# Kernel tuning notes

Hardware: AMD Instinct MI355X
Metric: run time of the kernel (lower is better)

Reference implementation:

```python
import jax, jax.numpy as jnp
import numpy as np

NUM_LAYER = 5
EMB = 64
ATOM_F = 32
BOND_F = 16
N_NODES = 50000
N_EDGES = 800000


def mish(x):
    return x * jnp.tanh(jax.nn.softplus(x))


def setup_inputs() -> dict:
    key = jax.random.key(0)
    ks = jax.random.split(key, 12)
    x = jax.random.normal(ks[0], (N_NODES, ATOM_F), dtype=jnp.float32)
    edge_index = jax.random.randint(ks[1], (2, N_EDGES), 0, N_NODES, dtype=jnp.int32)
    edge_attr = jax.random.normal(ks[2], (N_EDGES, BOND_F), dtype=jnp.float32)
    s = 0.05
    Wemb = jax.random.normal(ks[3], (EMB, ATOM_F), dtype=jnp.float32) * s
    W1 = jax.random.normal(ks[4], (NUM_LAYER, 2 * EMB, EMB), dtype=jnp.float32) * s
    b1 = jnp.zeros((NUM_LAYER, 2 * EMB), dtype=jnp.float32)
    W2 = jax.random.normal(ks[5], (NUM_LAYER, EMB, 2 * EMB), dtype=jnp.float32) * s
    b2 = jnp.zeros((NUM_LAYER, EMB), dtype=jnp.float32)
    We = jax.random.normal(ks[6], (NUM_LAYER, EMB, BOND_F), dtype=jnp.float32) * s
    be = jnp.zeros((NUM_LAYER, EMB), dtype=jnp.float32)
    gamma = jnp.ones((NUM_LAYER, EMB), dtype=jnp.float32)
    beta = jnp.zeros((NUM_LAYER, EMB), dtype=jnp.float32)
    return {"x": x, "edge_attr": edge_attr, "Wemb": Wemb, "W1": W1, "b1": b1,
            "W2": W2, "b2": b2, "We": We, "be": be, "gamma": gamma,
            "beta": beta, "edge_index": edge_index}


def reference(x, edge_attr, Wemb, W1, b1, W2, b2, We, be, gamma, beta, edge_index):
    N = x.shape[0]
    num_layer = W1.shape[0]
    # x_embedding: Linear(atom_feat, emb, bias=False)
    h = x @ Wemb.T  # [N, EMB]
    # add self loops once (edge_index is identical per layer in the module)
    loop = jnp.arange(N, dtype=edge_index.dtype)
    src = jnp.concatenate([edge_index[0], loop])  # message source (x_j)
    dst = jnp.concatenate([edge_index[1], loop])  # aggregation target
    # self-loop edge_attr is zeros
    ea_full = jnp.concatenate(
        [edge_attr, jnp.zeros((N, edge_attr.shape[1]), edge_attr.dtype)], axis=0)
    for l in range(num_layer):
        # GINConv: edge embedding + gather + scatter-add + MLP
        ee = ea_full @ We[l].T + be[l]          # [E+N, EMB]
        msg = h[src] + ee                        # x_j + edge_attr
        aggr = jax.ops.segment_sum(msg, dst, num_segments=N)  # aggr='add'
        hid = jax.nn.relu(aggr @ W1[l].T + b1[l])
        hn = hid @ W2[l].T + b2[l]
        # BatchNorm1d (training mode: batch statistics, biased variance)
        mu = hn.mean(axis=0)
        var = hn.var(axis=0)
        hn = (hn - mu) * jax.lax.rsqrt(var + 1e-5) * gamma[l] + beta[l]
        # mish on all but last layer; drop_ratio=0 so dropout is identity
        if l < num_layer - 1:
            hn = mish(hn)
        h = hn
    # JK='last'
    return h
```

## Files before the change

kernel.cpp:

```cpp
#include <hip/hip_runtime.h>

#define EMB 64
#define HID 128
#define BONDF 16
#define ATOMF 32

typedef __attribute__((ext_vector_type(8))) short short8v;
typedef __attribute__((ext_vector_type(16))) float f32x16;

__device__ __forceinline__ unsigned short f32_to_bf16_rne(float f) {
  unsigned u = __float_as_uint(f);
  u = (u + 0x7FFFu + ((u >> 16) & 1u)) >> 16;
  return (unsigned short)u;
}

__global__ __launch_bounds__(256) void embed_kernel(
    const float* __restrict__ x, const float* __restrict__ Wemb,
    float* __restrict__ h, int N)
{
  __shared__ float sW[EMB * ATOMF];
  int tid = threadIdx.x;
  for (int i = tid; i < EMB * ATOMF; i += 256) sW[i] = Wemb[i];
  __syncthreads();
  int row = blockIdx.x * 256 + tid;
  if (row >= N) return;
  float xin[ATOMF];
  const float4* xr = reinterpret_cast<const float4*>(x + (size_t)row * ATOMF);
#pragma unroll
  for (int k4 = 0; k4 < ATOMF / 4; ++k4) {
    float4 v = xr[k4];
    xin[4 * k4 + 0] = v.x; xin[4 * k4 + 1] = v.y;
    xin[4 * k4 + 2] = v.z; xin[4 * k4 + 3] = v.w;
  }
  float4* hr = reinterpret_cast<float4*>(h + (size_t)row * EMB);
  for (int o4 = 0; o4 < EMB / 4; ++o4) {
    float acc[4];
#pragma unroll
    for (int c = 0; c < 4; ++c) {
      const float* wrow = sW + (o4 * 4 + c) * ATOMF;
      float a = 0.f;
#pragma unroll
      for (int kk = 0; kk < ATOMF / 4; ++kk) {
        float4 w = reinterpret_cast<const float4*>(wrow)[kk];
        a = fmaf(w.x, xin[4 * kk + 0], a);
        a = fmaf(w.y, xin[4 * kk + 1], a);
        a = fmaf(w.z, xin[4 * kk + 2], a);
        a = fmaf(w.w, xin[4 * kk + 3], a);
      }
      acc[c] = a;
    }
    hr[o4] = make_float4(acc[0], acc[1], acc[2], acc[3]);
  }
}

__global__ __launch_bounds__(256) void cvt_bf16_kernel(
    const float* __restrict__ s, unsigned short* __restrict__ d, int n)
{
  int i = blockIdx.x * 256 + threadIdx.x;
  if (i < n) d[i] = f32_to_bf16_rne(s[i]);
}

__global__ __launch_bounds__(256) void deg_kernel(
    const int* __restrict__ ei, int* __restrict__ deg, int E)
{
  int e = blockIdx.x * 256 + threadIdx.x;
  if (e < E) atomicAdd(&deg[ei[E + e]], 1);
}

__global__ __launch_bounds__(256) void scan1_kernel(
    const int* __restrict__ deg, int* __restrict__ off,
    int* __restrict__ bsum, int n)
{
  __shared__ int ws[4];
  int tid = threadIdx.x, lane = tid & 63, wid = tid >> 6;
  int i = blockIdx.x * 256 + tid;
  int v = (i < n) ? deg[i] : 0;
  int x = v;
#pragma unroll
  for (int d = 1; d < 64; d <<= 1) {
    int t = __shfl_up(x, d, 64);
    if (lane >= d) x += t;
  }
  if (lane == 63) ws[wid] = x;
  __syncthreads();
  int add = 0;
  for (int w = 0; w < wid; ++w) add += ws[w];
  if (i < n) off[i] = x + add - v;
  if (tid == 255) bsum[blockIdx.x] = x + add;
}

__global__ __launch_bounds__(256) void scan_small_kernel(
    const int* __restrict__ deg, int* __restrict__ off, int n)
{
  __shared__ int warpsums[4];
  __shared__ int s_carry;
  int tid = threadIdx.x, lane = tid & 63, wid = tid >> 6;
  if (tid == 0) s_carry = 0;
  __syncthreads();
  for (int base = 0; base < n; base += 256) {
    int i = base + tid;
    int v = (i < n) ? deg[i] : 0;
    int x = v;
#pragma unroll
    for (int d = 1; d < 64; d <<= 1) {
      int t = __shfl_up(x, d, 64);
      if (lane >= d) x += t;
    }
    if (lane == 63) warpsums[wid] = x;
    __syncthreads();
    int wsum = 0;
    for (int w = 0; w < wid; ++w) wsum += warpsums[w];
    int incl = x + wsum + s_carry;
    if (i < n) off[i] = incl - v;
    __syncthreads();
    if (tid == 255) s_carry = incl;
    __syncthreads();
  }
  if (tid == 0) off[n] = s_carry;
}

__global__ __launch_bounds__(256) void scan3_kernel(
    int* __restrict__ off, const int* __restrict__ boff, int n)
{
  int i = blockIdx.x * 256 + threadIdx.x;
  if (i < n) off[i] += boff[blockIdx.x];
  if (i == 0) off[n] = boff[gridDim.x];
}

__global__ __launch_bounds__(256) void place_kernel(
    const int* __restrict__ ei, const int* __restrict__ off,
    int* __restrict__ cursor, int2* __restrict__ csr_packed, int E)
{
  int e = blockIdx.x * 256 + threadIdx.x;
  if (e >= E) return;
  int d = ei[E + e];
  int pos = atomicAdd(&cursor[d], 1);
  csr_packed[off[d] + pos] = make_int2(ei[e], e);
}

__global__ __launch_bounds__(256) void gather_ea_kernel(
    const float* __restrict__ ea, const int* __restrict__ off,
    const int2* __restrict__ csr_packed, float* __restrict__ S_ea, int N)
{
  int f = threadIdx.x & 15;
  int node = blockIdx.x * 16 + (threadIdx.x >> 4);
  if (node >= N) return;
  float acc = 0.f;
  int s0 = off[node], s1 = off[node + 1];
  int e = s0;
  if (e < s1 && (e & 1)) {
    acc += ea[(size_t)csr_packed[e].y * BONDF + f];
    ++e;
  }
  for (; e + 3 < s1; e += 4) {
    int4 p0 = *reinterpret_cast<const int4*>(csr_packed + e);
    int4 p1 = *reinterpret_cast<const int4*>(csr_packed + e + 2);
    float v0 = ea[(size_t)p0.y * BONDF + f];
    float v1 = ea[(size_t)p0.w * BONDF + f];
    float v2 = ea[(size_t)p1.y * BONDF + f];
    float v3 = ea[(size_t)p1.w * BONDF + f];
    acc += v0; acc += v1; acc += v2; acc += v3;
  }
  for (; e < s1; ++e)
    acc += ea[(size_t)csr_packed[e].y * BONDF + f];
  S_ea[(size_t)node * BONDF + f] = acc;
}

#define WEP (EMB + 1)
__global__ __launch_bounds__(256) void aggregate_ea_kernel(
    const float* __restrict__ h, const int* __restrict__ off,
    const int2* __restrict__ csr_packed, const float* __restrict__ S_ea,
    const float* __restrict__ We_l, const float* __restrict__ be_l,
    unsigned short* __restrict__ aggr16, int N)
{
  __shared__ float sWet[BONDF * WEP];
  __shared__ float sbe[EMB];
  int tid = threadIdx.x;
  for (int i = tid; i < EMB * BONDF; i += 256) {
    int k = i >> 4, f = i & 15;
    sWet[f * WEP + k] = We_l[i];
  }
  if (tid < EMB) sbe[tid] = be_l[tid];
  __syncthreads();
  int lane = tid & 63;
  int node = blockIdx.x * 4 + (tid >> 6);
  if (node >= N) return;
  float acc = h[(size_t)node * EMB + lane];
  int s0 = off[node], s1 = off[node + 1];
  int e = s0;
  if (e < s1 && (e & 1)) {
    acc += h[(size_t)csr_packed[e].x * EMB + lane];
    ++e;
  }
  for (; e + 15 < s1; e += 16) {
    int4 p0 = *reinterpret_cast<const int4*>(csr_packed + e);
    int4 p1 = *reinterpret_cast<const int4*>(csr_packed + e + 2);
    int4 p2 = *reinterpret_cast<const int4*>(csr_packed + e + 4);
    int4 p3 = *reinterpret_cast<const int4*>(csr_packed + e + 6);
    int4 p4 = *reinterpret_cast<const int4*>(csr_packed + e + 8);
    int4 p5 = *reinterpret_cast<const int4*>(csr_packed + e + 10);
    int4 p6 = *reinterpret_cast<const int4*>(csr_packed + e + 12);
    int4 p7 = *reinterpret_cast<const int4*>(csr_packed + e + 14);
    float v0  = h[(size_t)p0.x * EMB + lane];
    float v1  = h[(size_t)p0.z * EMB + lane];
    float v2  = h[(size_t)p1.x * EMB + lane];
    float v3  = h[(size_t)p1.z * EMB + lane];
    float v4  = h[(size_t)p2.x * EMB + lane];
    float v5  = h[(size_t)p2.z * EMB + lane];
    float v6  = h[(size_t)p3.x * EMB + lane];
    float v7  = h[(size_t)p3.z * EMB + lane];
    float v8  = h[(size_t)p4.x * EMB + lane];
    float v9  = h[(size_t)p4.z * EMB + lane];
    float v10 = h[(size_t)p5.x * EMB + lane];
    float v11 = h[(size_t)p5.z * EMB + lane];
    float v12 = h[(size_t)p6.x * EMB + lane];
    float v13 = h[(size_t)p6.z * EMB + lane];
    float v14 = h[(size_t)p7.x * EMB + lane];
    float v15 = h[(size_t)p7.z * EMB + lane];
    acc += v0;  acc += v1;  acc += v2;  acc += v3;
    acc += v4;  acc += v5;  acc += v6;  acc += v7;
    acc += v8;  acc += v9;  acc += v10; acc += v11;
    acc += v12; acc += v13; acc += v14; acc += v15;
  }
  for (; e + 1 < s1; e += 2) {
    int4 p = *reinterpret_cast<const int4*>(csr_packed + e);
    float v0 = h[(size_t)p.x * EMB + lane];
    float v1 = h[(size_t)p.z * EMB + lane];
    acc += v0; acc += v1;
  }
  if (e < s1) acc += h[(size_t)csr_packed[e].x * EMB + lane];
  float dp1 = (float)(s1 - s0) + 1.0f;
  acc = fmaf(sbe[lane], dp1, acc);
  const float* sea = S_ea + (size_t)node * BONDF;
#pragma unroll
  for (int f = 0; f < BONDF; ++f)
    acc = fmaf(sWet[f * WEP + lane], sea[f], acc);
  aggr16[(size_t)node * EMB + lane] = f32_to_bf16_rne(acc);
}

__global__ __launch_bounds__(256) void mlp_mfma_kernel(
    const unsigned short* __restrict__ aggr16,
    const unsigned short* __restrict__ W1b,
    const unsigned short* __restrict__ W2b,
    const float* __restrict__ b1,
    float* __restrict__ tmp, int N)
{
  int wid = threadIdx.x >> 6;
  int lane = threadIdx.x & 63;
  int chunk = blockIdx.x * 4 + wid;
  int row0 = chunk * 32;
  if (row0 >= N) return;
  int col = lane & 31;
  int g = lane >> 5;
  int row = row0 + col;
  int rowc = min(row, N - 1);

  f32x16 acc1[4] = {};
#pragma unroll
  for (int kt = 0; kt < 4; ++kt) {
    short8v bfrag = *reinterpret_cast<const short8v*>(
        aggr16 + (size_t)rowc * EMB + kt * 16 + g * 8);
#pragma unroll
    for (int mt = 0; mt < 4; ++mt) {
      short8v afrag = *reinterpret_cast<const short8v*>(
          W1b + (size_t)(mt * 32 + col) * EMB + kt * 16 + g * 8);
      acc1[mt] = __builtin_amdgcn_mfma_f32_32x32x16_bf16(afrag, bfrag, acc1[mt], 0, 0, 0);
    }
  }

  unsigned u[32];
#pragma unroll
  for (int t = 0; t < 16; ++t) {
    const int mt = t >> 2, q = t & 3;
    float v0 = fmaxf(acc1[mt][4 * q + 0] + b1[mt * 32 + 8 * q + 4 * g + 0], 0.f);
    float v1 = fmaxf(acc1[mt][4 * q + 1] + b1[mt * 32 + 8 * q + 4 * g + 1], 0.f);
    float v2 = fmaxf(acc1[mt][4 * q + 2] + b1[mt * 32 + 8 * q + 4 * g + 2], 0.f);
    float v3 = fmaxf(acc1[mt][4 * q + 3] + b1[mt * 32 + 8 * q + 4 * g + 3], 0.f);
    asm("v_cvt_pk_bf16_f32 %0, %1, %2" : "=v"(u[2 * t + 0]) : "v"(v0), "v"(v1));
    asm("v_cvt_pk_bf16_f32 %0, %1, %2" : "=v"(u[2 * t + 1]) : "v"(v2), "v"(v3));
  }

  short8v b2f[8];
#pragma unroll
  for (int kt2 = 0; kt2 < 8; ++kt2) {
    unsigned e0 = u[4 * kt2 + 0], e1 = u[4 * kt2 + 1];
    unsigned o0 = u[4 * kt2 + 2], o1 = u[4 * kt2 + 3];
    unsigned pe0 = (unsigned)__shfl_xor((int)e0, 32, 64);
    unsigned pe1 = (unsigned)__shfl_xor((int)e1, 32, 64);
    unsigned po0 = (unsigned)__shfl_xor((int)o0, 32, 64);
    unsigned po1 = (unsigned)__shfl_xor((int)o1, 32, 64);
    union { unsigned w[4]; short8v v; } cvt;
    cvt.w[0] = (g == 0) ? e0 : po0;
    cvt.w[1] = (g == 0) ? e1 : po1;
    cvt.w[2] = (g == 0) ? pe0 : o0;
    cvt.w[3] = (g == 0) ? pe1 : o1;
    b2f[kt2] = cvt.v;
  }

  f32x16 acc2[2] = {};
#pragma unroll
  for (int kt2 = 0; kt2 < 8; ++kt2) {
#pragma unroll
    for (int mt2 = 0; mt2 < 2; ++mt2) {
      short8v a2 = *reinterpret_cast<const short8v*>(
          W2b + (size_t)(mt2 * 32 + col) * HID + kt2 * 16 + g * 8);
      acc2[mt2] = __builtin_amdgcn_mfma_f32_32x32x16_bf16(a2, b2f[kt2], acc2[mt2], 0, 0, 0);
    }
  }

  if (row < N) {
#pragma unroll
    for (int mt2 = 0; mt2 < 2; ++mt2)
#pragma unroll
      for (int r = 0; r < 16; ++r) {
        int o = mt2 * 32 + (r & 3) + 8 * (r >> 2) + 4 * g;
        tmp[(size_t)row * EMB + o] = acc2[mt2][r];
      }
  }
}

__global__ __launch_bounds__(256) void stats_kernel(
    const float* __restrict__ tmp, float* __restrict__ gsums, int N)
{
  __shared__ float sh[256], sh2[256];
  int tid = threadIdx.x;
  int c = tid & 63, rg = tid >> 6;
  float s = 0.f, s2 = 0.f;
  for (int r = blockIdx.x * 4 + rg; r < N; r += gridDim.x * 4) {
    float v = tmp[(size_t)r * EMB + c];
    s += v; s2 += v * v;
  }
  sh[tid] = s; sh2[tid] = s2;
  __syncthreads();
  if (tid < 64) {
    s = sh[tid] + sh[tid + 64] + sh[tid + 128] + sh[tid + 192];
    s2 = sh2[tid] + sh2[tid + 64] + sh2[tid + 128] + sh2[tid + 192];
    atomicAdd(&gsums[c], s);
    atomicAdd(&gsums[EMB + c], s2);
  }
}

__global__ __launch_bounds__(256) void bn_kernel(
    const float* __restrict__ tmp, const float* __restrict__ gsums,
    const float* __restrict__ gamma, const float* __restrict__ beta,
    float* __restrict__ out, int N, int apply_mish)
{
  int idx = blockIdx.x * 256 + threadIdx.x;
  int total = N * (EMB / 4);
  if (idx >= total) return;
  int c4 = idx & (EMB / 4 - 1);
  float invN = 1.0f / (float)N;
  float4 v = reinterpret_cast<const float4*>(tmp)[idx];
  float o[4] = {v.x, v.y, v.z, v.w};
#pragma unroll
  for (int c = 0; c < 4; ++c) {
    int col = c4 * 4 + c;
    float mu = gsums[col] * invN;
    float var = gsums[EMB + col] * invN - mu * mu;
    float sc = gamma[col] * rsqrtf(var + 1e-5f);
    float shf = beta[col] - mu * sc;
    float y = o[c] * sc + shf;
    if (apply_mish) {
      float sp = (y > 20.f) ? y : log1pf(expf(y));
      y = y * tanhf(sp);
    }
    o[c] = y;
  }
  reinterpret_cast<float4*>(out)[idx] = make_float4(o[0], o[1], o[2], o[3]);
}

extern "C" void kernel_launch(void* const* d_in, const int* in_sizes, int n_in,
                              void* d_out, int out_size, void* d_ws, size_t ws_size,
                              hipStream_t stream) {
  (void)n_in; (void)out_size; (void)ws_size;
  const float* x     = (const float*)d_in[0];
  const float* ea    = (const float*)d_in[1];
  const float* Wemb  = (const float*)d_in[2];
  const float* W1    = (const float*)d_in[3];
  const float* b1    = (const float*)d_in[4];
  const float* W2    = (const float*)d_in[5];
  const float* We    = (const float*)d_in[7];
  const float* be    = (const float*)d_in[8];
  const float* gamma = (const float*)d_in[9];
  const float* beta  = (const float*)d_in[10];
  const int*   ei    = (const int*)d_in[11];

  int N = in_sizes[0] / ATOMF;
  int E = in_sizes[11] / 2;
  int L = in_sizes[3] / (HID * EMB);

  char* w = (char*)d_ws;
  auto alloc = [&](size_t bytes) {
    void* p = (void*)w;
    w += (bytes + 255) & ~(size_t)255;
    return p;
  };
  float*          h      = (float*)alloc((size_t)N * EMB * 4);
  float*          tmp    = (float*)alloc((size_t)N * EMB * 4);
  unsigned short* aggr16 = (unsigned short*)alloc((size_t)N * EMB * 2);
  float*          S_ea   = (float*)alloc((size_t)N * BONDF * 4);
  int*            deg    = (int*)alloc((size_t)N * 4);
  int*            off    = (int*)alloc((size_t)(N + 1) * 4);
  int*            cursor = (int*)alloc((size_t)N * 4);
  int2*           csrp   = (int2*)alloc((size_t)E * 8);
  int*            bsum   = (int*)alloc(1024 * 4);
  int*            boff   = (int*)alloc(1025 * 4);
  float*          gsums  = (float*)alloc(2 * EMB * 4);
  unsigned short* W1b    = (unsigned short*)alloc((size_t)L * HID * EMB * 2);
  unsigned short* W2b    = (unsigned short*)alloc((size_t)L * HID * EMB * 2);

  hipMemsetAsync(deg, 0, (size_t)N * 4, stream);
  hipMemsetAsync(cursor, 0, (size_t)N * 4, stream);

  int nW = L * HID * EMB;
  cvt_bf16_kernel<<<(nW + 255) / 256, 256, 0, stream>>>(W1, W1b, nW);
  cvt_bf16_kernel<<<(nW + 255) / 256, 256, 0, stream>>>(W2, W2b, nW);

  int nb = (N + 255) / 256;
  deg_kernel<<<(E + 255) / 256, 256, 0, stream>>>(ei, deg, E);
  scan1_kernel<<<nb, 256, 0, stream>>>(deg, off, bsum, N);
  scan_small_kernel<<<1, 256, 0, stream>>>(bsum, boff, nb);
  scan3_kernel<<<nb, 256, 0, stream>>>(off, boff, N);
  place_kernel<<<(E + 255) / 256, 256, 0, stream>>>(ei, off, cursor, csrp, E);
  gather_ea_kernel<<<(N + 15) / 16, 256, 0, stream>>>(ea, off, csrp, S_ea, N);
  embed_kernel<<<(N + 255) / 256, 256, 0, stream>>>(x, Wemb, h, N);

  int nchunk = (N + 31) / 32;
  for (int l = 0; l < L; ++l) {
    aggregate_ea_kernel<<<(N + 3) / 4, 256, 0, stream>>>(
        h, off, csrp, S_ea, We + (size_t)l * EMB * BONDF, be + (size_t)l * EMB,
        aggr16, N);
    mlp_mfma_kernel<<<(nchunk + 3) / 4, 256, 0, stream>>>(
        aggr16, W1b + (size_t)l * HID * EMB, W2b + (size_t)l * HID * EMB,
        b1 + (size_t)l * HID, tmp, N);
    hipMemsetAsync(gsums, 0, 2 * EMB * 4, stream);
    stats_kernel<<<512, 256, 0, stream>>>(tmp, gsums, N);
    float* outp = (l == L - 1) ? (float*)d_out : h;
    bn_kernel<<<(N * (EMB / 4) + 255) / 256, 256, 0, stream>>>(
        tmp, gsums, gamma + (size_t)l * EMB, beta + (size_t)l * EMB,
        outp, N, (l < L - 1) ? 1 : 0);
  }
}
```

Baseline: 740.2 us.

## Fuse BatchNorm statistics into MLP kernel and vectorize edge placement

Computes the per-column sum and sum-of-squares for BatchNorm inside the MFMA MLP kernel, using shared-memory atomics and then one global atomic per column per block. This removes the separate stats kernel and its re-read of tmp. It also replaces the per-layer memset with a single up-front memset of per-layer stat buffers, and merges the deg/cursor memsets into one. The place kernel now handles four edges per thread using int4 loads. The cost is heavy LDS atomic contention (many lanes add into the same 64 columns) and more global atomics, since each of the roughly 390 blocks adds its partial sums.

```diff
diff --git a/kernel.cpp b/kernel.cpp
--- a/kernel.cpp
+++ b/kernel.cpp
@@ -131,11 +131,27 @@
     const int* __restrict__ ei, const int* __restrict__ off,
     int* __restrict__ cursor, int2* __restrict__ csr_packed, int E)
 {
-  int e = blockIdx.x * 256 + threadIdx.x;
-  if (e >= E) return;
-  int d = ei[E + e];
-  int pos = atomicAdd(&cursor[d], 1);
-  csr_packed[off[d] + pos] = make_int2(ei[e], e);
+  int t = blockIdx.x * 256 + threadIdx.x;
+  int e0 = t * 4;
+  if (e0 >= E) return;
+  if (e0 + 3 < E) {
+    int4 s = *reinterpret_cast<const int4*>(ei + e0);
+    int4 d = *reinterpret_cast<const int4*>(ei + E + e0);
+    int p0 = atomicAdd(&cursor[d.x], 1);
+    int p1 = atomicAdd(&cursor[d.y], 1);
+    int p2 = atomicAdd(&cursor[d.z], 1);
+    int p3 = atomicAdd(&cursor[d.w], 1);
+    csr_packed[off[d.x] + p0] = make_int2(s.x, e0 + 0);
+    csr_packed[off[d.y] + p1] = make_int2(s.y, e0 + 1);
+    csr_packed[off[d.z] + p2] = make_int2(s.z, e0 + 2);
+    csr_packed[off[d.w] + p3] = make_int2(s.w, e0 + 3);
+  } else {
+    for (int e = e0; e < E; ++e) {
+      int d = ei[E + e];
+      int pos = atomicAdd(&cursor[d], 1);
+      csr_packed[off[d] + pos] = make_int2(ei[e], e);
+    }
+  }
 }
 
 __global__ __launch_bounds__(256) void gather_ea_kernel(
@@ -243,101 +259,93 @@
     const unsigned short* __restrict__ W1b,
     const unsigned short* __restrict__ W2b,
     const float* __restrict__ b1,
-    float* __restrict__ tmp, int N)
-{
-  int wid = threadIdx.x >> 6;
-  int lane = threadIdx.x & 63;
+    float* __restrict__ tmp, float* __restrict__ gsums_l, int N)
+{
+  __shared__ float sstat[2 * EMB];
+  int tid = threadIdx.x;
+  for (int i = tid; i < 2 * EMB; i += 256) sstat[i] = 0.f;
+  __syncthreads();
+
+  int wid = tid >> 6;
+  int lane = tid & 63;
   int chunk = blockIdx.x * 4 + wid;
   int row0 = chunk * 32;
-  if (row0 >= N) return;
-  int col = lane & 31;
-  int g = lane >> 5;
-  int row = row0 + col;
-  int rowc = min(row, N - 1);
-
-  f32x16 acc1[4] = {};
-#pragma unroll
-  for (int kt = 0; kt < 4; ++kt) {
-    short8v bfrag = *reinterpret_cast<const short8v*>(
-        aggr16 + (size_t)rowc * EMB + kt * 16 + g * 8);
-#pragma unroll
-    for (int mt = 0; mt < 4; ++mt) {
-      short8v afrag = *reinterpret_cast<const short8v*>(
-          W1b + (size_t)(mt * 32 + col) * EMB + kt * 16 + g * 8);
-      acc1[mt] = __builtin_amdgcn_mfma_f32_32x32x16_bf16(afrag, bfrag, acc1[mt], 0, 0, 0);
-    }
-  }
-
-  unsigned u[32];
-#pragma unroll
-  for (int t = 0; t < 16; ++t) {
-    const int mt = t >> 2, q = t & 3;
-    float v0 = fmaxf(acc1[mt][4 * q + 0] + b1[mt * 32 + 8 * q + 4 * g + 0], 0.f);
-    float v1 = fmaxf(acc1[mt][4 * q + 1] + b1[mt * 32 + 8 * q + 4 * g + 1], 0.f);
-    float v2 = fmaxf(acc1[mt][4 * q + 2] + b1[mt * 32 + 8 * q + 4 * g + 2], 0.f);
-    float v3 = fmaxf(acc1[mt][4 * q + 3] + b1[mt * 32 + 8 * q + 4 * g + 3], 0.f);
-    asm("v_cvt_pk_bf16_f32 %0, %1, %2" : "=v"(u[2 * t + 0]) : "v"(v0), "v"(v1));
-    asm("v_cvt_pk_bf16_f32 %0, %1, %2" : "=v"(u[2 * t + 1]) : "v"(v2), "v"(v3));
-  }
-
-  short8v b2f[8];
-#pragma unroll
-  for (int kt2 = 0; kt2 < 8; ++kt2) {
-    unsigned e0 = u[4 * kt2 + 0], e1 = u[4 * kt2 + 1];
-    unsigned o0 = u[4 * kt2 + 2], o1 = u[4 * kt2 + 3];
-    unsigned pe0 = (unsigned)__shfl_xor((int)e0, 32, 64);
-    unsigned pe1 = (unsigned)__shfl_xor((int)e1, 32, 64);
-    unsigned po0 = (unsigned)__shfl_xor((int)o0, 32, 64);
-    unsigned po1 = (unsigned)__shfl_xor((int)o1, 32, 64);
-    union { unsigned w[4]; short8v v; } cvt;
-    cvt.w[0] = (g == 0) ? e0 : po0;
-    cvt.w[1] = (g == 0) ? e1 : po1;
-    cvt.w[2] = (g == 0) ? pe0 : o0;
-    cvt.w[3] = (g == 0) ? pe1 : o1;
-    b2f[kt2] = cvt.v;
-  }
-
-  f32x16 acc2[2] = {};
-#pragma unroll
-  for (int kt2 = 0; kt2 < 8; ++kt2) {
-#pragma unroll
-    for (int mt2 = 0; mt2 < 2; ++mt2) {
-      short8v a2 = *reinterpret_cast<const short8v*>(
-          W2b + (size_t)(mt2 * 32 + col) * HID + kt2 * 16 + g * 8);
-      acc2[mt2] = __builtin_amdgcn_mfma_f32_32x32x16_bf16(a2, b2f[kt2], acc2[mt2], 0, 0, 0);
-    }
-  }
-
-  if (row < N) {
-#pragma unroll
-    for (int mt2 = 0; mt2 < 2; ++mt2)
-#pragma unroll
-      for (int r = 0; r < 16; ++r) {
-        int o = mt2 * 32 + (r & 3) + 8 * (r >> 2) + 4 * g;
-        tmp[(size_t)row * EMB + o] = acc2[mt2][r];
+  bool act = (row0 < N);
+  if (act) {
+    int col = lane & 31;
+    int g = lane >> 5;
+    int row = row0 + col;
+    int rowc = min(row, N - 1);
+
+    f32x16 acc1[4] = {};
+#pragma unroll
+    for (int kt = 0; kt < 4; ++kt) {
+      short8v bfrag = *reinterpret_cast<const short8v*>(
+          aggr16 + (size_t)rowc * EMB + kt * 16 + g * 8);
+#pragma unroll
+      for (int mt = 0; mt < 4; ++mt) {
+        short8v afrag = *reinterpret_cast<const short8v*>(
+            W1b + (size_t)(mt * 32 + col) * EMB + kt * 16 + g * 8);
+        acc1[mt] = __builtin_amdgcn_mfma_f32_32x32x16_bf16(afrag, bfrag, acc1[mt], 0, 0, 0);
       }
-  }
-}
-
-__global__ __launch_bounds__(256) void stats_kernel(
-    const float* __restrict__ tmp, float* __restrict__ gsums, int N)
-{
-  __shared__ float sh[256], sh2[256];
-  int tid = threadIdx.x;
-  int c = tid & 63, rg = tid >> 6;
-  float s = 0.f, s2 = 0.f;
-  for (int r = blockIdx.x * 4 + rg; r < N; r += gridDim.x * 4) {
-    float v = tmp[(size_t)r * EMB + c];
-    s += v; s2 += v * v;
-  }
-  sh[tid] = s; sh2[tid] = s2;
-  __syncthreads();
-  if (tid < 64) {
-    s = sh[tid] + sh[tid + 64] + sh[tid + 128] + sh[tid + 192];
-    s2 = sh2[tid] + sh2[tid + 64] + sh2[tid + 128] + sh2[tid + 192];
-    atomicAdd(&gsums[c], s);
-    atomicAdd(&gsums[EMB + c], s2);
-  }
+    }
+
+    unsigned u[32];
+#pragma unroll
+    for (int t = 0; t < 16; ++t) {
+      const int mt = t >> 2, q = t & 3;
+      float v0 = fmaxf(acc1[mt][4 * q + 0] + b1[mt * 32 + 8 * q + 4 * g + 0], 0.f);
+      float v1 = fmaxf(acc1[mt][4 * q + 1] + b1[mt * 32 + 8 * q + 4 * g + 1], 0.f);
+      float v2 = fmaxf(acc1[mt][4 * q + 2] + b1[mt * 32 + 8 * q + 4 * g + 2], 0.f);
+      float v3 = fmaxf(acc1[mt][4 * q + 3] + b1[mt * 32 + 8 * q + 4 * g + 3], 0.f);
+      asm("v_cvt_pk_bf16_f32 %0, %1, %2" : "=v"(u[2 * t + 0]) : "v"(v0), "v"(v1));
+      asm("v_cvt_pk_bf16_f32 %0, %1, %2" : "=v"(u[2 * t + 1]) : "v"(v2), "v"(v3));
+    }
+
+    short8v b2f[8];
+#pragma unroll
+    for (int kt2 = 0; kt2 < 8; ++kt2) {
+      unsigned e0 = u[4 * kt2 + 0], e1 = u[4 * kt2 + 1];
+      unsigned o0 = u[4 * kt2 + 2], o1 = u[4 * kt2 + 3];
+      unsigned pe0 = (unsigned)__shfl_xor((int)e0, 32, 64);
+      unsigned pe1 = (unsigned)__shfl_xor((int)e1, 32, 64);
+      unsigned po0 = (unsigned)__shfl_xor((int)o0, 32, 64);
+      unsigned po1 = (unsigned)__shfl_xor((int)o1, 32, 64);
+      union { unsigned w[4]; short8v v; } cvt;
+      cvt.w[0] = (g == 0) ? e0 : po0;
+      cvt.w[1] = (g == 0) ? e1 : po1;
+      cvt.w[2] = (g == 0) ? pe0 : o0;
+      cvt.w[3] = (g == 0) ? pe1 : o1;
+      b2f[kt2] = cvt.v;
+    }
+
+    f32x16 acc2[2] = {};
+#pragma unroll
+    for (int kt2 = 0; kt2 < 8; ++kt2) {
+#pragma unroll
+      for (int mt2 = 0; mt2 < 2; ++mt2) {
+        short8v a2 = *reinterpret_cast<const short8v*>(
+            W2b + (size_t)(mt2 * 32 + col) * HID + kt2 * 16 + g * 8);
+        acc2[mt2] = __builtin_amdgcn_mfma_f32_32x32x16_bf16(a2, b2f[kt2], acc2[mt2], 0, 0, 0);
+      }
+    }
+
+    if (row < N) {
+#pragma unroll
+      for (int mt2 = 0; mt2 < 2; ++mt2)
+#pragma unroll
+        for (int r = 0; r < 16; ++r) {
+          int o = mt2 * 32 + (r & 3) + 8 * (r >> 2) + 4 * g;
+          float v = acc2[mt2][r];
+          tmp[(size_t)row * EMB + o] = v;
+          atomicAdd(&sstat[o], v);
+          atomicAdd(&sstat[EMB + o], v * v);
+        }
+    }
+  }
+  __syncthreads();
+  for (int i = tid; i < 2 * EMB; i += 256)
+    atomicAdd(&gsums_l[i], sstat[i]);
 }
 
 __global__ __launch_bounds__(256) void bn_kernel(
@@ -400,17 +408,17 @@
   unsigned short* aggr16 = (unsigned short*)alloc((size_t)N * EMB * 2);
   float*          S_ea   = (float*)alloc((size_t)N * BONDF * 4);
   int*            deg    = (int*)alloc((size_t)N * 4);
+  int*            cursor = (int*)alloc((size_t)N * 4);
   int*            off    = (int*)alloc((size_t)(N + 1) * 4);
-  int*            cursor = (int*)alloc((size_t)N * 4);
   int2*           csrp   = (int2*)alloc((size_t)E * 8);
   int*            bsum   = (int*)alloc(1024 * 4);
   int*            boff   = (int*)alloc(1025 * 4);
-  float*          gsums  = (float*)alloc(2 * EMB * 4);
+  float*          gsums  = (float*)alloc((size_t)8 * 2 * EMB * 4);
   unsigned short* W1b    = (unsigned short*)alloc((size_t)L * HID * EMB * 2);
   unsigned short* W2b    = (unsigned short*)alloc((size_t)L * HID * EMB * 2);
 
-  hipMemsetAsync(deg, 0, (size_t)N * 4, stream);
-  hipMemsetAsync(cursor, 0, (size_t)N * 4, stream);
+  hipMemsetAsync(deg, 0, (size_t)((char*)cursor - (char*)deg) + (size_t)N * 4, stream);
+  hipMemsetAsync(gsums, 0, (size_t)L * 2 * EMB * 4, stream);
 
   int nW = L * HID * EMB;
   cvt_bf16_kernel<<<(nW + 255) / 256, 256, 0, stream>>>(W1, W1b, nW);
@@ -421,7 +429,7 @@
   scan1_kernel<<<nb, 256, 0, stream>>>(deg, off, bsum, N);
   scan_small_kernel<<<1, 256, 0, stream>>>(bsum, boff, nb);
   scan3_kernel<<<nb, 256, 0, stream>>>(off, boff, N);
-  place_kernel<<<(E + 255) / 256, 256, 0, stream>>>(ei, off, cursor, csrp, E);
+  place_kernel<<<((E + 3) / 4 + 255) / 256, 256, 0, stream>>>(ei, off, cursor, csrp, E);
   gather_ea_kernel<<<(N + 15) / 16, 256, 0, stream>>>(ea, off, csrp, S_ea, N);
   embed_kernel<<<(N + 255) / 256, 256, 0, stream>>>(x, Wemb, h, N);
 
@@ -432,12 +440,10 @@
         aggr16, N);
     mlp_mfma_kernel<<<(nchunk + 3) / 4, 256, 0, stream>>>(
         aggr16, W1b + (size_t)l * HID * EMB, W2b + (size_t)l * HID * EMB,
-        b1 + (size_t)l * HID, tmp, N);
-    hipMemsetAsync(gsums, 0, 2 * EMB * 4, stream);
-    stats_kernel<<<512, 256, 0, stream>>>(tmp, gsums, N);
+        b1 + (size_t)l * HID, tmp, gsums + (size_t)l * 2 * EMB, N);
     float* outp = (l == L - 1) ? (float*)d_out : h;
     bn_kernel<<<(N * (EMB / 4) + 255) / 256, 256, 0, stream>>>(
-        tmp, gsums, gamma + (size_t)l * EMB, beta + (size_t)l * EMB,
-        outp, N, (l < L - 1) ? 1 : 0);
-  }
-}
+        tmp, gsums + (size_t)l * 2 * EMB, gamma + (size_t)l * EMB,
+        beta + (size_t)l * EMB, outp, N, (l < L - 1) ? 1 : 0);
+  }
+}
```

Result: slower. 933.6 us (+26.1%).
